# Kernel tuning notes

Hardware: AMD Instinct MI355X
Metric: run time of the kernel (lower is better)

Reference implementation:

```python
import jax, jax.numpy as jnp
import numpy as np

E, B, D_IN, D_HID, D_OUT, G_HID, K = 8, 4096, 1024, 2048, 1024, 128, 2
LAMBDA_BALANCE, LAMBDA_ENTROPY = 5.0, 0.1


def setup_inputs() -> dict:
    key = jax.random.key(0)
    ks = jax.random.split(key, 8)
    s = 0.02  # xavier-ish init scale
    rn = lambda k, shape: jax.random.normal(k, shape, jnp.float32) * s
    return {
        "x": jax.random.normal(ks[0], (B, D_IN), jnp.float32),
        # stacked expert MLP params (torch Linear stored as [in, out])
        "We1": rn(ks[1], (E, D_IN, D_HID)), "be1": jnp.zeros((E, D_HID), jnp.float32),
        "We2": rn(ks[2], (E, D_HID, D_HID)), "be2": jnp.zeros((E, D_HID), jnp.float32),
        "We3": rn(ks[3], (E, D_HID, D_OUT)), "be3": jnp.zeros((E, D_OUT), jnp.float32),
        # gate MLP params
        "Wg1": rn(ks[4], (D_IN, G_HID)), "bg1": jnp.zeros((G_HID,), jnp.float32),
        "Wg2": rn(ks[5], (G_HID, G_HID)), "bg2": jnp.zeros((G_HID,), jnp.float32),
        "Wg3": rn(ks[6], (G_HID, E)), "bg3": jnp.zeros((E,), jnp.float32),
    }


def reference(x, We1, be1, We2, be2, We3, be3, Wg1, bg1, Wg2, bg2, Wg3, bg3):
    # ---- gate MLP -> softmax -> top-k routing ----
    g = jax.nn.relu(x @ Wg1 + bg1)
    g = jax.nn.relu(g @ Wg2 + bg2)
    logits = g @ Wg3 + bg3                     # [B, E]
    gate_scores = jax.nn.softmax(logits, axis=1)
    top_k_scores, top_k_indices = jax.lax.top_k(gate_scores, K)  # [B, K]

    # ---- all-expert dense MLP on the full batch (as in the torch module) ----
    h = jax.nn.relu(jnp.einsum('bi,eih->ebh', x, We1) + be1[:, None, :])
    h = jax.nn.relu(jnp.einsum('ebh,ehf->ebf', h, We2) + be2[:, None, :])
    expert_out = jnp.einsum('ebf,efo->ebo', h, We3) + be3[:, None, :]  # [E, B, D_OUT]
    expert_out = jnp.transpose(expert_out, (1, 0, 2))                  # [B, E, D_OUT]

    # ---- gather top-k, scale by gate score, normalize, combine ----
    sel = jnp.take_along_axis(expert_out, top_k_indices[:, :, None], axis=1)  # [B, K, D]
    denom = top_k_scores.sum(axis=1, keepdims=True)[:, :, None] + 1e-9
    combined = (sel * top_k_scores[:, :, None] / denom).sum(axis=1)           # [B, D]

    # ---- auxiliary loss (load balance variance + gate entropy) ----
    one_hot = jax.nn.one_hot(top_k_indices, E, dtype=jnp.float32)  # [B, K, E]
    expert_load = one_hot.sum(axis=(0, 1)) / (B + 1e-9)
    load_balancing_loss = jnp.var(expert_load, ddof=1)  # torch .var() is unbiased
    entropy = -(gate_scores * jnp.log(gate_scores + 1e-9)).sum(axis=1).mean()
    aux_loss = LAMBDA_BALANCE * load_balancing_loss + LAMBDA_ENTROPY * entropy

    return combined, aux_loss, top_k_indices, top_k_scores
```

## Files before the change

### kernel.cpp

```cpp
#include <hip/hip_runtime.h>
#include <stdint.h>
#include <stddef.h>

#define E_ 8
#define B_ 4096
#define DIN 1024
#define DHID 2048
#define DOUT 1024

#define RMAX 9216
#define NTILES 72

#define OUT_AUX  4194304
#define OUT_IDX  4194305
#define OUT_SC   4202497

using f32x4  = __attribute__((ext_vector_type(4))) float;
using bf16x8 = __attribute__((ext_vector_type(8))) short;

static __device__ __forceinline__ unsigned short f2bf(float f) {
  unsigned int u = __builtin_bit_cast(unsigned int, f);
  u += 0x7FFFu + ((u >> 16) & 1u);
  return (unsigned short)(u >> 16);
}

#define GLOAD_LDS(gp, lp) __builtin_amdgcn_global_load_lds( \
    (const __attribute__((address_space(1))) void*)(gp),    \
    (__attribute__((address_space(3))) void*)(lp), 16, 0, 0)

__global__ void k_init(int* counts, int* cnt2, float* esum) {
  int t = threadIdx.x;
  if (t < E_) { counts[t] = 0; cnt2[t] = 0; }
  if (t == 0) esum[0] = 0.f;
}

__global__ void k_conv(const float* __restrict__ W, unsigned short* __restrict__ Wt,
                       int K, int N) {
  __shared__ float tile[32][33];
  const int e = blockIdx.z;
  const float* We = W + (size_t)e * K * N;
  unsigned short* Wte = Wt + (size_t)e * N * K;
  const int k0 = blockIdx.x * 32, n0 = blockIdx.y * 32;
  const int tx = threadIdx.x, ty = threadIdx.y;
  #pragma unroll
  for (int j = 0; j < 32; j += 8)
    tile[ty + j][tx] = We[(size_t)(k0 + ty + j) * N + n0 + tx];
  __syncthreads();
  #pragma unroll
  for (int j = 0; j < 32; j += 8)
    Wte[(size_t)(n0 + ty + j) * K + k0 + tx] = f2bf(tile[tx][ty + j]);
}

__global__ __launch_bounds__(256) void k_gate(
    const float* __restrict__ x,
    const float* __restrict__ Wg1, const float* __restrict__ bg1,
    const float* __restrict__ Wg2, const float* __restrict__ bg2,
    const float* __restrict__ Wg3, const float* __restrict__ bg3,
    float* __restrict__ dout, int* __restrict__ counts, float* __restrict__ esum)
{
  __shared__ __align__(16) float xs[16][1024];
  __shared__ __align__(16) float g1s[16][128];
  __shared__ __align__(16) float g2s[16][128];
  __shared__ float ls[16][8];
  const int t = threadIdx.x;
  const int b0 = blockIdx.x * 16;

  {
    const f32x4* xg = (const f32x4*)(x + (size_t)b0 * DIN);
    f32x4* xl = (f32x4*)&xs[0][0];
    #pragma unroll
    for (int i = 0; i < 16; i++) xl[t + i * 256] = xg[t + i * 256];
  }
  __syncthreads();

  const int w = t >> 6, l = t & 63;
  const int r0 = w * 4;
  double a0[4], a1[4];

  {
    const double bA = (double)bg1[l], bB = (double)bg1[64 + l];
    #pragma unroll
    for (int r = 0; r < 4; r++) { a0[r] = bA; a1[r] = bB; }
    for (int i = 0; i < 1024; i += 4) {
      f32x4 xv[4];
      #pragma unroll
      for (int r = 0; r < 4; r++) xv[r] = *(const f32x4*)&xs[r0 + r][i];
      #pragma unroll
      for (int q = 0; q < 4; q++) {
        const double w0 = (double)Wg1[(size_t)(i + q) * 128 + l];
        const double w1 = (double)Wg1[(size_t)(i + q) * 128 + 64 + l];
        #pragma unroll
        for (int r = 0; r < 4; r++) {
          a0[r] += (double)xv[r][q] * w0;
          a1[r] += (double)xv[r][q] * w1;
        }
      }
    }
    #pragma unroll
    for (int r = 0; r < 4; r++) {
      g1s[r0 + r][l]      = fmaxf((float)a0[r], 0.f);
      g1s[r0 + r][64 + l] = fmaxf((float)a1[r], 0.f);
    }
  }
  __syncthreads();

  {
    const double bA = (double)bg2[l], bB = (double)bg2[64 + l];
    #pragma unroll
    for (int r = 0; r < 4; r++) { a0[r] = bA; a1[r] = bB; }
    for (int j = 0; j < 128; j += 4) {
      f32x4 gv[4];
      #pragma unroll
      for (int r = 0; r < 4; r++) gv[r] = *(const f32x4*)&g1s[r0 + r][j];
      #pragma unroll
      for (int q = 0; q < 4; q++) {
        const double w0 = (double)Wg2[(size_t)(j + q) * 128 + l];
        const double w1 = (double)Wg2[(size_t)(j + q) * 128 + 64 + l];
        #pragma unroll
        for (int r = 0; r < 4; r++) {
          a0[r] += (double)gv[r][q] * w0;
          a1[r] += (double)gv[r][q] * w1;
        }
      }
    }
    #pragma unroll
    for (int r = 0; r < 4; r++) {
      g2s[r0 + r][l]      = fmaxf((float)a0[r], 0.f);
      g2s[r0 + r][64 + l] = fmaxf((float)a1[r], 0.f);
    }
  }
  __syncthreads();

  if (t < 128) {
    const int r = t >> 3, e = t & 7;
    double a = (double)bg3[e];
    for (int j = 0; j < 128; j++)
      a += (double)g2s[r][j] * (double)Wg3[j * 8 + e];
    ls[r][e] = (float)a;
  }
  __syncthreads();

  if (t < 16) {
    const int b = b0 + t;
    float lg[8], p[8];
    float m = -3.4e38f;
    #pragma unroll
    for (int e = 0; e < 8; e++) { lg[e] = ls[t][e]; m = fmaxf(m, lg[e]); }
    float s = 0.f;
    #pragma unroll
    for (int e = 0; e < 8; e++) { p[e] = expf(lg[e] - m); s += p[e]; }
    #pragma unroll
    for (int e = 0; e < 8; e++) p[e] = p[e] / s;
    int i0 = 0;
    #pragma unroll
    for (int e = 1; e < 8; e++) if (p[e] > p[i0]) i0 = e;
    int i1 = (i0 == 0) ? 1 : 0;
    #pragma unroll
    for (int e = 0; e < 8; e++) if (e != i0 && p[e] > p[i1]) i1 = e;
    float ent = 0.f;
    #pragma unroll
    for (int e = 0; e < 8; e++) ent -= p[e] * logf(p[e] + 1e-9f);
    dout[OUT_IDX + (size_t)b * 2 + 0] = (float)i0;
    dout[OUT_IDX + (size_t)b * 2 + 1] = (float)i1;
    dout[OUT_SC  + (size_t)b * 2 + 0] = p[i0];
    dout[OUT_SC  + (size_t)b * 2 + 1] = p[i1];
    atomicAdd(&counts[i0], 1);
    atomicAdd(&counts[i1], 1);
    atomicAdd(esum, ent);
  }
}

__global__ void k_offsets(const int* __restrict__ counts, int* __restrict__ seg,
                          int* __restrict__ tilee, const float* __restrict__ esum,
                          float* __restrict__ dout) {
  if (threadIdx.x != 0 || blockIdx.x != 0) return;
  for (int t = 0; t < NTILES; t++) tilee[t] = -1;
  int s = 0;
  float loads[E_];
  float mean = 0.f;
  for (int e = 0; e < E_; e++) {
    const int c = counts[e];
    seg[e] = s;
    const int tiles = (c + 127) >> 7;
    for (int lt = 0; lt < tiles; lt++) tilee[(s >> 7) + lt] = e;
    s += tiles << 7;
    loads[e] = (float)c / 4096.0f;
    mean += loads[e];
  }
  seg[E_] = s;
  mean *= 0.125f;
  float var = 0.f;
  for (int e = 0; e < E_; e++) { const float d = loads[e] - mean; var += d * d; }
  var /= 7.0f;
  dout[OUT_AUX] = 5.0f * var + 0.1f * (esum[0] / 4096.0f);
}

__global__ void k_scatter(const float* __restrict__ dout, int* __restrict__ posmap,
                          float* __restrict__ wgt, int* __restrict__ cnt2,
                          const int* __restrict__ seg) {
  const int a = blockIdx.x * 256 + threadIdx.x;
  if (a >= B_ * 2) return;
  const int b = a >> 1;
  const int e = (int)dout[OUT_IDX + a];
  const float sc = dout[OUT_SC + a];
  const float denom = dout[OUT_SC + b * 2] + dout[OUT_SC + b * 2 + 1] + 1e-9f;
  const int p = seg[e] + atomicAdd(&cnt2[e], 1);
  posmap[a] = p;
  wgt[p] = sc / denom;
}

__global__ void k_gather(const float* __restrict__ x, const int* __restrict__ posmap,
                         unsigned short* __restrict__ Xg) {
  const int a = blockIdx.x, t = threadIdx.x;
  const int b = a >> 1;
  const int p = posmap[a];
  const f32x4* xr = (const f32x4*)(x + (size_t)b * DIN);
  const f32x4 v0 = xr[t * 2], v1 = xr[t * 2 + 1];
  bf16x8 s;
  s[0] = (short)f2bf(v0[0]); s[1] = (short)f2bf(v0[1]);
  s[2] = (short)f2bf(v0[2]); s[3] = (short)f2bf(v0[3]);
  s[4] = (short)f2bf(v1[0]); s[5] = (short)f2bf(v1[1]);
  s[6] = (short)f2bf(v1[2]); s[7] = (short)f2bf(v1[3]);
  ((bf16x8*)(Xg + (size_t)p * DIN))[t] = s;
}

template<bool RELU, bool OUTF32>
__global__ __launch_bounds__(256) void k_gemm(
    const unsigned short* __restrict__ A, int lda,
    const unsigned short* __restrict__ Wt,
    const float* __restrict__ bias,
    void* __restrict__ Cv, int N, int K,
    const int* __restrict__ tilee)
{
  const int e = tilee[blockIdx.x];
  if (e < 0) return;
  __shared__ __align__(16) unsigned short As[128 * 32];
  __shared__ __align__(16) unsigned short Bs[128 * 32];
  const int tid = threadIdx.x;
  const int m0 = blockIdx.x * 128;
  const int n0 = blockIdx.y * 128;
  const unsigned short* __restrict__ Ab = A + (size_t)m0 * lda;
  const unsigned short* __restrict__ Bb = Wt + (size_t)e * N * K + (size_t)n0 * K;

  const int c0 = tid, c1 = tid + 256;
  const int ar0 = c0 >> 2, ak0 = (c0 & 3) * 8;
  const int ar1 = c1 >> 2, ak1 = (c1 & 3) * 8;

  const int lane = tid & 63;
  const int wid  = tid >> 6;
  const int wm = wid >> 1, wn = wid & 1;
  const int fr = lane & 15, g = lane >> 4;

  const f32x4 zero = {0.f, 0.f, 0.f, 0.f};
  f32x4 acc[4][4];
  #pragma unroll
  for (int m = 0; m < 4; m++)
    #pragma unroll
    for (int n = 0; n < 4; n++) acc[m][n] = zero;

  const bf16x8* As8 = (const bf16x8*)As;
  const bf16x8* Bs8 = (const bf16x8*)Bs;

  for (int k0 = 0; k0 < K; k0 += 32) {
    GLOAD_LDS(Ab + (size_t)ar0 * lda + k0 + ak0, &As[c0 * 8]);
    GLOAD_LDS(Ab + (size_t)ar1 * lda + k0 + ak1, &As[c1 * 8]);
    GLOAD_LDS(Bb + (size_t)ar0 * K   + k0 + ak0, &Bs[c0 * 8]);
    GLOAD_LDS(Bb + (size_t)ar1 * K   + k0 + ak1, &Bs[c1 * 8]);
    __syncthreads();
    bf16x8 av[4], bv[4];
    #pragma unroll
    for (int m = 0; m < 4; m++) av[m] = As8[(wm * 64 + m * 16 + fr) * 4 + g];
    #pragma unroll
    for (int n = 0; n < 4; n++) bv[n] = Bs8[(wn * 64 + n * 16 + fr) * 4 + g];
    __syncthreads();
    #pragma unroll
    for (int m = 0; m < 4; m++)
      #pragma unroll
      for (int n = 0; n < 4; n++)
        acc[m][n] = __builtin_amdgcn_mfma_f32_16x16x32_bf16(av[m], bv[n], acc[m][n], 0, 0, 0);
  }

  float* Cf = (float*)Cv;
  unsigned short* Ch = (unsigned short*)Cv;
  #pragma unroll
  for (int n = 0; n < 4; n++) {
    const int col = n0 + wn * 64 + n * 16 + fr;
    const float bvv = bias[(size_t)e * N + col];
    #pragma unroll
    for (int m = 0; m < 4; m++) {
      const int row = m0 + wm * 64 + m * 16 + g * 4;
      #pragma unroll
      for (int r = 0; r < 4; r++) {
        float v = acc[m][n][r] + bvv;
        if (RELU) v = fmaxf(v, 0.f);
        if (OUTF32) Cf[(size_t)(row + r) * N + col] = v;
        else        Ch[(size_t)(row + r) * N + col] = f2bf(v);
      }
    }
  }
}

__global__ void k_combine(const float* __restrict__ Yg, const int* __restrict__ posmap,
                          const float* __restrict__ wgt, float* __restrict__ out) {
  const int b = blockIdx.x, t = threadIdx.x;
  const int p0 = posmap[b * 2], p1 = posmap[b * 2 + 1];
  const float w0 = wgt[p0], w1 = wgt[p1];
  const f32x4 y0 = ((const f32x4*)(Yg + (size_t)p0 * DOUT))[t];
  const f32x4 y1 = ((const f32x4*)(Yg + (size_t)p1 * DOUT))[t];
  f32x4 o = y0 * w0 + y1 * w1;
  ((f32x4*)(out + (size_t)b * DOUT))[t] = o;
}

extern "C" void kernel_launch(void* const* d_in, const int* in_sizes, int n_in,
                              void* d_out, int out_size, void* d_ws, size_t ws_size,
                              hipStream_t stream) {
  (void)in_sizes; (void)n_in; (void)out_size; (void)ws_size;
  const float* x   = (const float*)d_in[0];
  const float* We1 = (const float*)d_in[1];
  const float* be1 = (const float*)d_in[2];
  const float* We2 = (const float*)d_in[3];
  const float* be2 = (const float*)d_in[4];
  const float* We3 = (const float*)d_in[5];
  const float* be3 = (const float*)d_in[6];
  const float* Wg1 = (const float*)d_in[7];
  const float* bg1 = (const float*)d_in[8];
  const float* Wg2 = (const float*)d_in[9];
  const float* bg2 = (const float*)d_in[10];
  const float* Wg3 = (const float*)d_in[11];
  const float* bg3 = (const float*)d_in[12];
  float* out = (float*)d_out;

  char* ws = (char*)d_ws;
  size_t off = 0;
  auto alloc = [&](size_t bytes) {
    char* p = ws + off;
    off += (bytes + 255) & ~(size_t)255;
    return p;
  };
  unsigned short* WT1 = (unsigned short*)alloc((size_t)E_ * DHID * DIN * 2);
  unsigned short* WT2 = (unsigned short*)alloc((size_t)E_ * DHID * DHID * 2);
  unsigned short* WT3 = (unsigned short*)alloc((size_t)E_ * DOUT * DHID * 2);
  unsigned short* XG  = (unsigned short*)alloc((size_t)RMAX * DIN * 2);
  unsigned short* H1  = (unsigned short*)alloc((size_t)RMAX * DHID * 2);
  unsigned short* H2  = (unsigned short*)alloc((size_t)RMAX * DHID * 2);
  int*   posmap = (int*)alloc((size_t)B_ * 2 * 4);
  float* wgt    = (float*)alloc((size_t)RMAX * 4);
  int*   counts = (int*)alloc(256);
  int*   cnt2   = (int*)alloc(256);
  int*   seg    = (int*)alloc(256);
  int*   tilee  = (int*)alloc(512);
  float* esum   = (float*)alloc(256);
  float* Yg = (float*)H1;

  k_init<<<1, 64, 0, stream>>>(counts, cnt2, esum);
  k_conv<<<dim3(DIN / 32, DHID / 32, E_), dim3(32, 8), 0, stream>>>(We1, WT1, DIN, DHID);
  k_conv<<<dim3(DHID / 32, DHID / 32, E_), dim3(32, 8), 0, stream>>>(We2, WT2, DHID, DHID);
  k_conv<<<dim3(DHID / 32, DOUT / 32, E_), dim3(32, 8), 0, stream>>>(We3, WT3, DHID, DOUT);
  k_gate<<<B_ / 16, 256, 0, stream>>>(x, Wg1, bg1, Wg2, bg2, Wg3, bg3, out, counts, esum);
  k_offsets<<<1, 1, 0, stream>>>(counts, seg, tilee, esum, out);
  k_scatter<<<(B_ * 2) / 256, 256, 0, stream>>>(out, posmap, wgt, cnt2, seg);
  k_gather<<<B_ * 2, 128, 0, stream>>>(x, posmap, XG);
  k_gemm<true,  false><<<dim3(NTILES, DHID / 128), 256, 0, stream>>>(XG, DIN,  WT1, be1, (void*)H1, DHID, DIN,  tilee);
  k_gemm<true,  false><<<dim3(NTILES, DHID / 128), 256, 0, stream>>>(H1, DHID, WT2, be2, (void*)H2, DHID, DHID, tilee);
  k_gemm<false, true ><<<dim3(NTILES, DOUT / 128), 256, 0, stream>>>(H2, DHID, WT3, be3, (void*)Yg, DOUT, DHID, tilee);
  k_combine<<<B_, 256, 0, stream>>>(Yg, posmap, wgt, out);
}
```

Baseline: 854.0 us.

## Widen weight-transpose stores and spread gate MLP over more blocks

The weight conversion kernel now transposes 64x32 tiles and writes two packed bf16 values per 32-bit store instead of one 16-bit store per thread. The gate kernel now handles 4 rows per block instead of 16, which launches four times as many blocks. It pre-converts x to double in shared memory and gives each thread one output column for two rows. The intent is to cut the double-precision gate stage's long serial per-block work and its poor occupancy, at the cost of reloading the gate weights in more blocks.

```diff
diff --git a/kernel.cpp b/kernel.cpp
--- a/kernel.cpp
+++ b/kernel.cpp
@@ -36,19 +36,23 @@
 
 __global__ void k_conv(const float* __restrict__ W, unsigned short* __restrict__ Wt,
                        int K, int N) {
-  __shared__ float tile[32][33];
+  __shared__ float tile[64][33];
   const int e = blockIdx.z;
   const float* We = W + (size_t)e * K * N;
   unsigned short* Wte = Wt + (size_t)e * N * K;
-  const int k0 = blockIdx.x * 32, n0 = blockIdx.y * 32;
+  const int k0 = blockIdx.x * 64, n0 = blockIdx.y * 32;
   const int tx = threadIdx.x, ty = threadIdx.y;
   #pragma unroll
-  for (int j = 0; j < 32; j += 8)
+  for (int j = 0; j < 64; j += 8)
     tile[ty + j][tx] = We[(size_t)(k0 + ty + j) * N + n0 + tx];
   __syncthreads();
   #pragma unroll
-  for (int j = 0; j < 32; j += 8)
-    Wte[(size_t)(n0 + ty + j) * K + k0 + tx] = f2bf(tile[tx][ty + j]);
+  for (int j = 0; j < 32; j += 8) {
+    const int n = ty + j;
+    const unsigned int lo = f2bf(tile[2 * tx][n]);
+    const unsigned int hi = f2bf(tile[2 * tx + 1][n]);
+    *(unsigned int*)&Wte[(size_t)(n0 + n) * K + k0 + 2 * tx] = lo | (hi << 16);
+  }
 }
 
 __global__ __launch_bounds__(256) void k_gate(
@@ -58,80 +62,70 @@
     const float* __restrict__ Wg3, const float* __restrict__ bg3,
     float* __restrict__ dout, int* __restrict__ counts, float* __restrict__ esum)
 {
-  __shared__ __align__(16) float xs[16][1024];
-  __shared__ __align__(16) float g1s[16][128];
-  __shared__ __align__(16) float g2s[16][128];
-  __shared__ float ls[16][8];
+  __shared__ __align__(16) double xs[4][1024];
+  __shared__ __align__(16) float g1s[4][128];
+  __shared__ __align__(16) float g2s[4][128];
+  __shared__ float ls[4][8];
   const int t = threadIdx.x;
-  const int b0 = blockIdx.x * 16;
+  const int b0 = blockIdx.x * 4;
 
   {
-    const f32x4* xg = (const f32x4*)(x + (size_t)b0 * DIN);
-    f32x4* xl = (f32x4*)&xs[0][0];
-    #pragma unroll
-    for (int i = 0; i < 16; i++) xl[t + i * 256] = xg[t + i * 256];
-  }
-  __syncthreads();
-
-  const int w = t >> 6, l = t & 63;
-  const int r0 = w * 4;
-  double a0[4], a1[4];
+    const float2* xg = (const float2*)(x + (size_t)b0 * DIN);
+    double2* xl = (double2*)&xs[0][0];
+    #pragma unroll
+    for (int i = 0; i < 8; i++) {
+      const float2 v = xg[t + i * 256];
+      double2 d; d.x = (double)v.x; d.y = (double)v.y;
+      xl[t + i * 256] = d;
+    }
+  }
+  __syncthreads();
+
+  const int c = t & 127, rr = t >> 7;
 
   {
-    const double bA = (double)bg1[l], bB = (double)bg1[64 + l];
-    #pragma unroll
-    for (int r = 0; r < 4; r++) { a0[r] = bA; a1[r] = bB; }
+    double a0 = (double)bg1[c], a1 = a0;
+    const float* wp = Wg1 + c;
     for (int i = 0; i < 1024; i += 4) {
-      f32x4 xv[4];
-      #pragma unroll
-      for (int r = 0; r < 4; r++) xv[r] = *(const f32x4*)&xs[r0 + r][i];
-      #pragma unroll
-      for (int q = 0; q < 4; q++) {
-        const double w0 = (double)Wg1[(size_t)(i + q) * 128 + l];
-        const double w1 = (double)Wg1[(size_t)(i + q) * 128 + 64 + l];
-        #pragma unroll
-        for (int r = 0; r < 4; r++) {
-          a0[r] += (double)xv[r][q] * w0;
-          a1[r] += (double)xv[r][q] * w1;
-        }
-      }
+      const float w0 = wp[(size_t)(i + 0) * 128];
+      const float w1 = wp[(size_t)(i + 1) * 128];
+      const float w2 = wp[(size_t)(i + 2) * 128];
+      const float w3 = wp[(size_t)(i + 3) * 128];
+      const double2* xr0 = (const double2*)&xs[rr][i];
+      const double2* xr2 = (const double2*)&xs[rr + 2][i];
+      const double2 xa = xr0[0], xb = xr0[1];
+      const double2 xc = xr2[0], xd = xr2[1];
+      a0 += (double)w0 * xa.x; a1 += (double)w0 * xc.x;
+      a0 += (double)w1 * xa.y; a1 += (double)w1 * xc.y;
+      a0 += (double)w2 * xb.x; a1 += (double)w2 * xd.x;
+      a0 += (double)w3 * xb.y; a1 += (double)w3 * xd.y;
     }
-    #pragma unroll
-    for (int r = 0; r < 4; r++) {
-      g1s[r0 + r][l]      = fmaxf((float)a0[r], 0.f);
-      g1s[r0 + r][64 + l] = fmaxf((float)a1[r], 0.f);
+    g1s[rr][c]     = fmaxf((float)a0, 0.f);
+    g1s[rr + 2][c] = fmaxf((float)a1, 0.f);
+  }
+  __syncthreads();
+
+  {
+    double a0 = (double)bg2[c], a1 = a0;
+    const float* wp = Wg2 + c;
+    for (int j = 0; j < 128; j += 4) {
+      const float w0 = wp[(size_t)(j + 0) * 128];
+      const float w1 = wp[(size_t)(j + 1) * 128];
+      const float w2 = wp[(size_t)(j + 2) * 128];
+      const float w3 = wp[(size_t)(j + 3) * 128];
+      const f32x4 ga = *(const f32x4*)&g1s[rr][j];
+      const f32x4 gb = *(const f32x4*)&g1s[rr + 2][j];
+      a0 += (double)w0 * (double)ga[0]; a1 += (double)w0 * (double)gb[0];
+      a0 += (double)w1 * (double)ga[1]; a1 += (double)w1 * (double)gb[1];
+      a0 += (double)w2 * (double)ga[2]; a1 += (double)w2 * (double)gb[2];
+      a0 += (double)w3 * (double)ga[3]; a1 += (double)w3 * (double)gb[3];
     }
-  }
-  __syncthreads();
-
-  {
-    const double bA = (double)bg2[l], bB = (double)bg2[64 + l];
-    #pragma unroll
-    for (int r = 0; r < 4; r++) { a0[r] = bA; a1[r] = bB; }
-    for (int j = 0; j < 128; j += 4) {
-      f32x4 gv[4];
-      #pragma unroll
-      for (int r = 0; r < 4; r++) gv[r] = *(const f32x4*)&g1s[r0 + r][j];
-      #pragma unroll
-      for (int q = 0; q < 4; q++) {
-        const double w0 = (double)Wg2[(size_t)(j + q) * 128 + l];
-        const double w1 = (double)Wg2[(size_t)(j + q) * 128 + 64 + l];
-        #pragma unroll
-        for (int r = 0; r < 4; r++) {
-          a0[r] += (double)gv[r][q] * w0;
-          a1[r] += (double)gv[r][q] * w1;
-        }
-      }
-    }
-    #pragma unroll
-    for (int r = 0; r < 4; r++) {
-      g2s[r0 + r][l]      = fmaxf((float)a0[r], 0.f);
-      g2s[r0 + r][64 + l] = fmaxf((float)a1[r], 0.f);
-    }
-  }
-  __syncthreads();
-
-  if (t < 128) {
+    g2s[rr][c]     = fmaxf((float)a0, 0.f);
+    g2s[rr + 2][c] = fmaxf((float)a1, 0.f);
+  }
+  __syncthreads();
+
+  if (t < 32) {
     const int r = t >> 3, e = t & 7;
     double a = (double)bg3[e];
     for (int j = 0; j < 128; j++)
@@ -140,7 +134,7 @@
   }
   __syncthreads();
 
-  if (t < 16) {
+  if (t < 4) {
     const int b = b0 + t;
     float lg[8], p[8];
     float m = -3.4e38f;
@@ -353,10 +347,10 @@
   float* Yg = (float*)H1;
 
   k_init<<<1, 64, 0, stream>>>(counts, cnt2, esum);
-  k_conv<<<dim3(DIN / 32, DHID / 32, E_), dim3(32, 8), 0, stream>>>(We1, WT1, DIN, DHID);
-  k_conv<<<dim3(DHID / 32, DHID / 32, E_), dim3(32, 8), 0, stream>>>(We2, WT2, DHID, DHID);
-  k_conv<<<dim3(DHID / 32, DOUT / 32, E_), dim3(32, 8), 0, stream>>>(We3, WT3, DHID, DOUT);
-  k_gate<<<B_ / 16, 256, 0, stream>>>(x, Wg1, bg1, Wg2, bg2, Wg3, bg3, out, counts, esum);
+  k_conv<<<dim3(DIN / 64, DHID / 32, E_), dim3(32, 8), 0, stream>>>(We1, WT1, DIN, DHID);
+  k_conv<<<dim3(DHID / 64, DHID / 32, E_), dim3(32, 8), 0, stream>>>(We2, WT2, DHID, DHID);
+  k_conv<<<dim3(DHID / 64, DOUT / 32, E_), dim3(32, 8), 0, stream>>>(We3, WT3, DHID, DOUT);
+  k_gate<<<B_ / 4, 256, 0, stream>>>(x, Wg1, bg1, Wg2, bg2, Wg3, bg3, out, counts, esum);
   k_offsets<<<1, 1, 0, stream>>>(counts, seg, tilee, esum, out);
   k_scatter<<<(B_ * 2) / 256, 256, 0, stream>>>(out, posmap, wgt, cnt2, seg);
   k_gather<<<B_ * 2, 128, 0, stream>>>(x, posmap, XG);
```

Result: faster. 755.0 us (-11.6%).
